# Performance work log

Hardware: AMD Instinct MI355X
Metric: run time of the kernel (lower is better)

Reference implementation:

```python
import jax, jax.numpy as jnp
import numpy as np

B, S, D, O, C = 4, 2048, 1024, 1024, 8


def setup_inputs() -> dict:
    key = jax.random.key(0)
    k1, k2, k3, k4 = jax.random.split(key, 4)
    x = jax.random.normal(k1, (B, S, D), dtype=jnp.float32)
    category_id = jax.random.randint(k2, (B, S), 0, C, dtype=jnp.int64)
    weight = jax.random.normal(k3, (C, D, O), dtype=jnp.float32)
    bias = jax.random.normal(k4, (C, O), dtype=jnp.float32)
    return {"x": x, "category_id": category_id, "weight": weight, "bias": bias}


def reference(x, category_id, weight, bias):
    # Faithful to: out[t] = x[t] @ weight[cid[t]] + bias[cid[t]]
    # Instead of gathering a full [T, D, O] weight tensor per token (32GB),
    # compute every category's projection once and select per token.
    orig_shape = x.shape
    x_flat = x.reshape(-1, orig_shape[-1])          # [T, D]
    cid = category_id.reshape(-1)                    # [T]
    out_all = jnp.einsum('td,cdo->tco', x_flat, weight)  # [T, C, O]
    out = jnp.take_along_axis(out_all, cid[:, None, None], axis=1)[:, 0, :]  # [T, O]
    out = out + bias[cid]
    return out.reshape(orig_shape[:-1] + (weight.shape[-1],))
```

## Files before the change

### kernel.cpp

```cpp
#include <hip/hip_runtime.h>

#define TOK   8192
#define DIM   1024
#define OUTD  1024
#define NCAT  8
#define BM    128
#define BN    128
#define BK    32
#define MAX_MT 71
#define MPMAX (MAX_MT * BM)

typedef __attribute__((ext_vector_type(8))) __bf16 bf16x8;
typedef __attribute__((ext_vector_type(4))) float  f32x4;

__device__ __forceinline__ unsigned short f2bf(float f) {
  unsigned u = __float_as_uint(f);
  u += 0x7fffu + ((u >> 16) & 1u);
  return (unsigned short)(u >> 16);
}

__global__ __launch_bounds__(1024) void k_build(const int* __restrict__ cid,
    int* __restrict__ row_token, int* __restrict__ tile_c, int* __restrict__ tile_m) {
  __shared__ int wcnt[16][NCAT];
  __shared__ int wbase[16][NCAT];
  __shared__ int gbase[NCAT];
  int tid = threadIdx.x, lane = tid & 63, wave = tid >> 6;
  int base = wave * 512;

  int cs[8];
  #pragma unroll
  for (int it = 0; it < 8; ++it) cs[it] = cid[base + it * 64 + lane];
  int cnt_loc[NCAT];
  #pragma unroll
  for (int c = 0; c < NCAT; ++c) cnt_loc[c] = 0;
  #pragma unroll
  for (int it = 0; it < 8; ++it) {
    #pragma unroll
    for (int c = 0; c < NCAT; ++c) {
      unsigned long long m = __ballot(cs[it] == c);
      cnt_loc[c] += __popcll(m);
    }
  }
  if (lane == 0) {
    #pragma unroll
    for (int c = 0; c < NCAT; ++c) wcnt[wave][c] = cnt_loc[c];
  }
  __syncthreads();

  if (tid == 0) {
    int pr = 0, mt = 0;
    for (int c = 0; c < NCAT; ++c) {
      int tot = 0;
      for (int w = 0; w < 16; ++w) { wbase[w][c] = tot; tot += wcnt[w][c]; }
      gbase[c] = pr;
      int nt = (tot + BM - 1) / BM;
      for (int i = 0; i < nt; ++i) { tile_c[mt] = c; tile_m[mt] = pr + i * BM; ++mt; }
      pr += nt * BM;
    }
    for (; mt < MAX_MT; ++mt) { tile_c[mt] = -1; tile_m[mt] = 0; }
  }
  __syncthreads();
  for (int r = tid; r < MPMAX; r += 1024) row_token[r] = -1;
  __syncthreads();

  int run[NCAT];
  #pragma unroll
  for (int c = 0; c < NCAT; ++c) run[c] = gbase[c] + wbase[wave][c];
  unsigned long long lt = (lane == 63) ? ~0ull >> 1 : ((1ull << lane) - 1);
  #pragma unroll
  for (int it = 0; it < 8; ++it) {
    int t = base + it * 64 + lane;
    int c = cs[it];
    int pos = 0;
    #pragma unroll
    for (int cat = 0; cat < NCAT; ++cat) {
      unsigned long long m = __ballot(cs[it] == cat);
      if (cat == c) pos = run[cat] + __popcll(m & lt);
      run[cat] += __popcll(m);
    }
    row_token[pos] = t;
  }
}

__global__ __launch_bounds__(256) void k_convert(const float* __restrict__ w,
    const float* __restrict__ x, const int* __restrict__ row_token,
    unsigned short* __restrict__ wt, unsigned short* __restrict__ xg) {
  int tid = threadIdx.x;
  if (blockIdx.x < 2048) {
    int b = blockIdx.x;
    int ot = b & 15, dt = (b >> 4) & 15, c = b >> 8;
    __shared__ unsigned short t[64][72];
    int i  = tid >> 2;
    int jg = tid & 3;
    const float* src = w + ((size_t)c << 20) + (size_t)(dt * 64 + i) * 1024 + ot * 64 + jg * 16;
    #pragma unroll
    for (int q = 0; q < 4; ++q) {
      float4 v = *(const float4*)(src + q * 4);
      t[jg * 16 + q * 4 + 0][i] = f2bf(v.x);
      t[jg * 16 + q * 4 + 1][i] = f2bf(v.y);
      t[jg * 16 + q * 4 + 2][i] = f2bf(v.z);
      t[jg * 16 + q * 4 + 3][i] = f2bf(v.w);
    }
    __syncthreads();
    unsigned short* dst = wt + ((size_t)c << 20) + (size_t)(ot * 64 + i) * 1024 + dt * 64 + jg * 16;
    uint4 a = *(const uint4*)&t[i][jg * 16];
    uint4 bq = *(const uint4*)&t[i][jg * 16 + 8];
    *(uint4*)dst = a;
    *(uint4*)(dst + 8) = bq;
  } else {
    int idx = (blockIdx.x - 2048) * 256 + tid;
    int r  = idx >> 7;
    int e0 = (idx & 127) << 3;
    if (r >= MPMAX) return;
    int tok = row_token[r];
    union { unsigned short u[8]; uint4 v; } o;
    if (tok >= 0) {
      const float4* s = (const float4*)(x + (size_t)tok * DIM + e0);
      float4 a = s[0], b = s[1];
      o.u[0] = f2bf(a.x); o.u[1] = f2bf(a.y); o.u[2] = f2bf(a.z); o.u[3] = f2bf(a.w);
      o.u[4] = f2bf(b.x); o.u[5] = f2bf(b.y); o.u[6] = f2bf(b.z); o.u[7] = f2bf(b.w);
    } else {
      o.v = make_uint4(0u, 0u, 0u, 0u);
    }
    *(uint4*)(xg + (size_t)r * DIM + e0) = o.v;
  }
}

__global__ __launch_bounds__(256) void k_gemm(const unsigned short* __restrict__ xg,
    const unsigned short* __restrict__ wt, const float* __restrict__ bias,
    const int* __restrict__ row_token, const int* __restrict__ tile_c,
    const int* __restrict__ tile_m, float* __restrict__ out) {
  int mt = blockIdx.y;
  int c = tile_c[mt];
  if (c < 0) return;
  int m0 = tile_m[mt];
  int n0 = blockIdx.x * BN;

  __shared__ unsigned short As[2][BM][BK];
  __shared__ unsigned short Bs[2][BM][BK];

  int tid  = threadIdx.x;
  int lane = tid & 63;
  int wave = tid >> 6;
  int wr = wave >> 1, wc = wave & 1;

  f32x4 acc[4][4];
  #pragma unroll
  for (int m = 0; m < 4; ++m)
    #pragma unroll
    for (int n = 0; n < 4; ++n) acc[m][n] = (f32x4){0.f, 0.f, 0.f, 0.f};

  const unsigned short* Ag = xg + (size_t)m0 * DIM;
  const unsigned short* Bg = wt + ((size_t)c << 20) + (size_t)n0 * DIM;
  int srow = tid >> 2;
  int scol = (tid & 3) << 3;

  auto STAGE = [&](int buf, int kt) {
    __builtin_amdgcn_global_load_lds(
      (const __attribute__((address_space(1))) unsigned int*)(Ag + (size_t)srow * DIM + kt + scol),
      (__attribute__((address_space(3))) unsigned int*)(&As[buf][srow][scol]), 16, 0, 0);
    __builtin_amdgcn_global_load_lds(
      (const __attribute__((address_space(1))) unsigned int*)(Ag + (size_t)(srow + 64) * DIM + kt + scol),
      (__attribute__((address_space(3))) unsigned int*)(&As[buf][srow + 64][scol]), 16, 0, 0);
    __builtin_amdgcn_global_load_lds(
      (const __attribute__((address_space(1))) unsigned int*)(Bg + (size_t)srow * DIM + kt + scol),
      (__attribute__((address_space(3))) unsigned int*)(&Bs[buf][srow][scol]), 16, 0, 0);
    __builtin_amdgcn_global_load_lds(
      (const __attribute__((address_space(1))) unsigned int*)(Bg + (size_t)(srow + 64) * DIM + kt + scol),
      (__attribute__((address_space(3))) unsigned int*)(&Bs[buf][srow + 64][scol]), 16, 0, 0);
  };

  STAGE(0, 0);
  __syncthreads();

  int cur = 0;
  for (int kt = 0; kt < DIM - BK; kt += BK) {
    STAGE(cur ^ 1, kt + BK);
    bf16x8 a[4], b[4];
    #pragma unroll
    for (int m = 0; m < 4; ++m)
      a[m] = *(const bf16x8*)&As[cur][wr * 64 + m * 16 + (lane & 15)][(lane >> 4) * 8];
    #pragma unroll
    for (int n = 0; n < 4; ++n)
      b[n] = *(const bf16x8*)&Bs[cur][wc * 64 + n * 16 + (lane & 15)][(lane >> 4) * 8];
    #pragma unroll
    for (int m = 0; m < 4; ++m)
      #pragma unroll
      for (int n = 0; n < 4; ++n)
        acc[m][n] = __builtin_amdgcn_mfma_f32_16x16x32_bf16(a[m], b[n], acc[m][n], 0, 0, 0);
    __syncthreads();
    cur ^= 1;
  }
  {
    bf16x8 a[4], b[4];
    #pragma unroll
    for (int m = 0; m < 4; ++m)
      a[m] = *(const bf16x8*)&As[cur][wr * 64 + m * 16 + (lane & 15)][(lane >> 4) * 8];
    #pragma unroll
    for (int n = 0; n < 4; ++n)
      b[n] = *(const bf16x8*)&Bs[cur][wc * 64 + n * 16 + (lane & 15)][(lane >> 4) * 8];
    #pragma unroll
    for (int m = 0; m < 4; ++m)
      #pragma unroll
      for (int n = 0; n < 4; ++n)
        acc[m][n] = __builtin_amdgcn_mfma_f32_16x16x32_bf16(a[m], b[n], acc[m][n], 0, 0, 0);
  }

  int col = lane & 15;
  int rq  = (lane >> 4) << 2;
  float bv[4];
  #pragma unroll
  for (int n = 0; n < 4; ++n) bv[n] = bias[c * OUTD + n0 + wc * 64 + n * 16 + col];
  #pragma unroll
  for (int m = 0; m < 4; ++m) {
    #pragma unroll
    for (int r = 0; r < 4; ++r) {
      int prow = m0 + wr * 64 + m * 16 + rq + r;
      int tok = row_token[prow];
      if (tok < 0) continue;
      float* orow = out + (size_t)tok * OUTD + n0 + wc * 64 + col;
      #pragma unroll
      for (int n = 0; n < 4; ++n) orow[n * 16] = acc[m][n][r] + bv[n];
    }
  }
}

extern "C" void kernel_launch(void* const* d_in, const int* in_sizes, int n_in,
                              void* d_out, int out_size, void* d_ws, size_t ws_size,
                              hipStream_t stream) {
  const float* x    = (const float*)d_in[0];
  const int*   cid  = (const int*)d_in[1];
  const float* w    = (const float*)d_in[2];
  const float* bias = (const float*)d_in[3];
  float* out = (float*)d_out;

  char* ws = (char*)d_ws;
  constexpr size_t XG_BYTES = (size_t)MPMAX * DIM * 2;
  constexpr size_t WT_BYTES = (size_t)NCAT * DIM * OUTD * 2;
  constexpr size_t RT_BYTES = (size_t)MPMAX * 4;
  unsigned short* xg  = (unsigned short*)ws;
  unsigned short* wtb = (unsigned short*)(ws + XG_BYTES);
  int* row_token = (int*)(ws + XG_BYTES + WT_BYTES);
  int* tile_c    = (int*)(ws + XG_BYTES + WT_BYTES + RT_BYTES);
  int* tile_m    = tile_c + MAX_MT;

  k_build<<<1, 1024, 0, stream>>>(cid, row_token, tile_c, tile_m);
  k_convert<<<2048 + (MPMAX * (DIM / 8) + 255) / 256, 256, 0, stream>>>(w, x, row_token, wtb, xg);
  k_gemm<<<dim3(OUTD / BN, MAX_MT), 256, 0, stream>>>(xg, wtb, bias, row_token, tile_c, tile_m, out);
}
```

Measured before the change: 161.3 us.

## Triple-buffer GEMM loads, swizzle LDS layout, and remap workgroups across XCDs

The GEMM main loop moves from double to triple buffering. It uses explicit vmcnt waits and raw barriers so two stages of global-to-LDS loads stay in flight while MFMAs run. The column position of each 16-byte chunk is XOR-swizzled on the global-load side and un-swizzled on the read side to cut LDS bank conflicts. The grid is flattened to 1D and remapped so consecutive workgroups on each XCD share M-tiles, aiming for better L2 reuse. In exchange, LDS use rises by half and the code relies on hand-counted vmcnt values staying correct.

```diff
diff --git a/kernel.cpp b/kernel.cpp
--- a/kernel.cpp
+++ b/kernel.cpp
@@ -7,6 +7,7 @@
 #define BM    128
 #define BN    128
 #define BK    32
+#define NKT   (DIM / BK)
 #define MAX_MT 71
 #define MPMAX (MAX_MT * BM)
 
@@ -130,19 +131,21 @@
     const unsigned short* __restrict__ wt, const float* __restrict__ bias,
     const int* __restrict__ row_token, const int* __restrict__ tile_c,
     const int* __restrict__ tile_m, float* __restrict__ out) {
-  int mt = blockIdx.y;
+  int wg  = blockIdx.x;
+  int lin = (wg & 7) * MAX_MT + (wg >> 3);
+  int mt  = lin >> 3;
+  int nt  = lin & 7;
   int c = tile_c[mt];
   if (c < 0) return;
   int m0 = tile_m[mt];
-  int n0 = blockIdx.x * BN;
-
-  __shared__ unsigned short As[2][BM][BK];
-  __shared__ unsigned short Bs[2][BM][BK];
+  int n0 = nt * BN;
+
+  __shared__ unsigned short As[3][BM][BK];
+  __shared__ unsigned short Bs[3][BM][BK];
 
   int tid  = threadIdx.x;
   int lane = tid & 63;
-  int wave = tid >> 6;
-  int wr = wave >> 1, wc = wave & 1;
+  int wr = (tid >> 6) >> 1, wc = (tid >> 6) & 1;
 
   f32x4 acc[4][4];
   #pragma unroll
@@ -152,58 +155,55 @@
 
   const unsigned short* Ag = xg + (size_t)m0 * DIM;
   const unsigned short* Bg = wt + ((size_t)c << 20) + (size_t)n0 * DIM;
+
   int srow = tid >> 2;
-  int scol = (tid & 3) << 3;
-
-  auto STAGE = [&](int buf, int kt) {
-    __builtin_amdgcn_global_load_lds(
-      (const __attribute__((address_space(1))) unsigned int*)(Ag + (size_t)srow * DIM + kt + scol),
-      (__attribute__((address_space(3))) unsigned int*)(&As[buf][srow][scol]), 16, 0, 0);
-    __builtin_amdgcn_global_load_lds(
-      (const __attribute__((address_space(1))) unsigned int*)(Ag + (size_t)(srow + 64) * DIM + kt + scol),
-      (__attribute__((address_space(3))) unsigned int*)(&As[buf][srow + 64][scol]), 16, 0, 0);
-    __builtin_amdgcn_global_load_lds(
-      (const __attribute__((address_space(1))) unsigned int*)(Bg + (size_t)srow * DIM + kt + scol),
-      (__attribute__((address_space(3))) unsigned int*)(&Bs[buf][srow][scol]), 16, 0, 0);
-    __builtin_amdgcn_global_load_lds(
-      (const __attribute__((address_space(1))) unsigned int*)(Bg + (size_t)(srow + 64) * DIM + kt + scol),
-      (__attribute__((address_space(3))) unsigned int*)(&Bs[buf][srow + 64][scol]), 16, 0, 0);
+  int sdst = (tid & 3) << 3;
+  int gsrc = (((tid & 3) ^ ((tid >> 3) & 3)) << 3);
+
+  auto STAGE = [&](int b, int kt) {
+    __builtin_amdgcn_global_load_lds(
+      (const __attribute__((address_space(1))) unsigned int*)(Ag + (size_t)srow * DIM + kt + gsrc),
+      (__attribute__((address_space(3))) unsigned int*)(&As[b][srow][sdst]), 16, 0, 0);
+    __builtin_amdgcn_global_load_lds(
+      (const __attribute__((address_space(1))) unsigned int*)(Ag + (size_t)(srow + 64) * DIM + kt + gsrc),
+      (__attribute__((address_space(3))) unsigned int*)(&As[b][srow + 64][sdst]), 16, 0, 0);
+    __builtin_amdgcn_global_load_lds(
+      (const __attribute__((address_space(1))) unsigned int*)(Bg + (size_t)srow * DIM + kt + gsrc),
+      (__attribute__((address_space(3))) unsigned int*)(&Bs[b][srow][sdst]), 16, 0, 0);
+    __builtin_amdgcn_global_load_lds(
+      (const __attribute__((address_space(1))) unsigned int*)(Bg + (size_t)(srow + 64) * DIM + kt + gsrc),
+      (__attribute__((address_space(3))) unsigned int*)(&Bs[b][srow + 64][sdst]), 16, 0, 0);
   };
 
-  STAGE(0, 0);
-  __syncthreads();
-
-  int cur = 0;
-  for (int kt = 0; kt < DIM - BK; kt += BK) {
-    STAGE(cur ^ 1, kt + BK);
-    bf16x8 a[4], b[4];
+  int rcol = (((lane >> 4) ^ ((lane & 15) >> 1 & 3)) << 3);
+  int arow = wr * 64 + (lane & 15);
+  int brow = wc * 64 + (lane & 15);
+
+  STAGE(0, 0); STAGE(1, BK); STAGE(2, 2 * BK);
+
+  int b = 0;
+  for (int t = 0; t < NKT; ++t) {
+    if (t < NKT - 2)       asm volatile("s_waitcnt vmcnt(8)" ::: "memory");
+    else if (t == NKT - 2) asm volatile("s_waitcnt vmcnt(4)" ::: "memory");
+    else                   asm volatile("s_waitcnt vmcnt(0)" ::: "memory");
+    __builtin_amdgcn_s_barrier();
+
+    bf16x8 af[4], bf[4];
     #pragma unroll
     for (int m = 0; m < 4; ++m)
-      a[m] = *(const bf16x8*)&As[cur][wr * 64 + m * 16 + (lane & 15)][(lane >> 4) * 8];
+      af[m] = *(const bf16x8*)&As[b][arow + m * 16][rcol];
     #pragma unroll
     for (int n = 0; n < 4; ++n)
-      b[n] = *(const bf16x8*)&Bs[cur][wc * 64 + n * 16 + (lane & 15)][(lane >> 4) * 8];
+      bf[n] = *(const bf16x8*)&Bs[b][brow + n * 16][rcol];
     #pragma unroll
     for (int m = 0; m < 4; ++m)
       #pragma unroll
       for (int n = 0; n < 4; ++n)
-        acc[m][n] = __builtin_amdgcn_mfma_f32_16x16x32_bf16(a[m], b[n], acc[m][n], 0, 0, 0);
-    __syncthreads();
-    cur ^= 1;
-  }
-  {
-    bf16x8 a[4], b[4];
-    #pragma unroll
-    for (int m = 0; m < 4; ++m)
-      a[m] = *(const bf16x8*)&As[cur][wr * 64 + m * 16 + (lane & 15)][(lane >> 4) * 8];
-    #pragma unroll
-    for (int n = 0; n < 4; ++n)
-      b[n] = *(const bf16x8*)&Bs[cur][wc * 64 + n * 16 + (lane & 15)][(lane >> 4) * 8];
-    #pragma unroll
-    for (int m = 0; m < 4; ++m)
-      #pragma unroll
-      for (int n = 0; n < 4; ++n)
-        acc[m][n] = __builtin_amdgcn_mfma_f32_16x16x32_bf16(a[m], b[n], acc[m][n], 0, 0, 0);
+        acc[m][n] = __builtin_amdgcn_mfma_f32_16x16x32_bf16(af[m], bf[n], acc[m][n], 0, 0, 0);
+
+    __builtin_amdgcn_s_barrier();
+    if (t < NKT - 3) STAGE(b, (t + 3) * BK);
+    b = (b == 2) ? 0 : b + 1;
   }
 
   int col = lane & 15;
@@ -246,5 +246,5 @@
 
   k_build<<<1, 1024, 0, stream>>>(cid, row_token, tile_c, tile_m);
   k_convert<<<2048 + (MPMAX * (DIM / 8) + 255) / 256, 256, 0, stream>>>(w, x, row_token, wtb, xg);
-  k_gemm<<<dim3(OUTD / BN, MAX_MT), 256, 0, stream>>>(xg, wtb, bias, row_token, tile_c, tile_m, out);
-}
+  k_gemm<<<8 * MAX_MT, 256, 0, stream>>>(xg, wtb, bias, row_token, tile_c, tile_m, out);
+}
```

Result: faster. 151.0 us (-6.4%).
